# Kernel optimization log

Measured on AMD Instinct MI355X. Metric: run time of the kernel, lower is better.

Reference implementation:

```python
import jax, jax.numpy as jnp
import numpy as np

NUM_HEADS = 16
BLOCK_KV = 64


def _split_heads(x, h):
    B, T, D = x.shape
    return x.reshape(B, T, h, D // h).transpose(0, 2, 1, 3)  # [B,H,T,Hd]


def _merge_heads(x):
    B, H, T, Hd = x.shape
    return x.transpose(0, 2, 1, 3).reshape(B, T, H * Hd)


def _streaming_attention(qh, kh, vh, bkv):
    # Online-softmax (flash-attention) over kv blocks; math identical to the
    # original nested-loop version (including the Z + 1e-9 denominator).
    B, H, T, Dh = qh.shape
    scale = 1.0 / jnp.sqrt(Dh).astype(jnp.float32)
    q32 = qh.astype(jnp.float32)
    nb = T // bkv
    # [nb, B, H, bkv, Dh]
    kb = jnp.moveaxis(kh.astype(jnp.float32).reshape(B, H, nb, bkv, Dh), 2, 0)
    vb = jnp.moveaxis(vh.astype(jnp.float32).reshape(B, H, nb, bkv, Dh), 2, 0)

    def step(carry, blk):
        m, Z, O = carry
        k_blk, v_blk = blk
        scores = jnp.einsum('bhtd,bhkd->bhtk', q32, k_blk) * scale
        m_new = jnp.maximum(m, jnp.max(scores, axis=-1, keepdims=True))
        alpha = jnp.exp(m - m_new)
        p = jnp.exp(scores - m_new)
        Z = Z * alpha + jnp.sum(p, axis=-1, keepdims=True)
        O = O * alpha + jnp.einsum('bhtk,bhkd->bhtd', p, v_blk)
        return (m_new, Z, O), None

    m0 = jnp.full((B, H, T, 1), -jnp.inf, dtype=jnp.float32)
    Z0 = jnp.zeros((B, H, T, 1), dtype=jnp.float32)
    O0 = jnp.zeros((B, H, T, Dh), dtype=jnp.float32)
    (m, Z, O), _ = jax.lax.scan(step, (m0, Z0, O0), (kb, vb))
    return (O / (Z + 1e-9)).astype(qh.dtype)


def setup_inputs() -> dict:
    key = jax.random.key(0)
    ks = jax.random.split(key, 6)
    B, T, D = 4, 8192, 512
    s = 1.0 / np.sqrt(D)
    return {
        'x': jax.random.normal(ks[0], (B, T, D), dtype=jnp.float32),
        'Wq': jax.random.normal(ks[1], (D, D), dtype=jnp.float32) * s,
        'Wk': jax.random.normal(ks[2], (D, D), dtype=jnp.float32) * s,
        'Wv': jax.random.normal(ks[3], (D, D), dtype=jnp.float32) * s,
        'Wo': jax.random.normal(ks[4], (D, D), dtype=jnp.float32) * s,
        'bo': jnp.zeros((D,), dtype=jnp.float32),
    }


def reference(x, Wq, Wk, Wv, Wo, bo):
    q = x @ Wq
    k = x @ Wk
    v = x @ Wv
    qh = _split_heads(q, NUM_HEADS)
    kh = _split_heads(k, NUM_HEADS)
    vh = _split_heads(v, NUM_HEADS)
    out_h = _streaming_attention(qh, kh, vh, BLOCK_KV)
    return _merge_heads(out_h) @ Wo + bo
```

## Files before the change

### kernel.cpp

```cpp
#include <hip/hip_runtime.h>
#include <hip/hip_bf16.h>
#include <math.h>

typedef __bf16 bf16;
typedef __bf16 bf16x2 __attribute__((ext_vector_type(2)));
typedef __bf16 bf16x4 __attribute__((ext_vector_type(4)));
typedef __bf16 bf16x8 __attribute__((ext_vector_type(8)));
typedef float f32x4 __attribute__((ext_vector_type(4)));
typedef unsigned int u32;
typedef u32 u32x4 __attribute__((ext_vector_type(4)));

#define B_ 4
#define T_ 8192
#define D_ 512
#define H_ 16
#define HD_ 32
#define M_ (B_ * T_)

#if __has_builtin(__builtin_amdgcn_exp2f)
#define EXP2(x) __builtin_amdgcn_exp2f(x)
#else
#define EXP2(x) exp2f(x)
#endif

#define LDSP(p) ((__attribute__((address_space(3))) void*)(p))
#define GLBP(p) ((const __attribute__((address_space(1))) void*)(p))

static __device__ __forceinline__ u32 pkbf16(float a, float b) {
  bf16x2 t;
  t[0] = (bf16)a;
  t[1] = (bf16)b;
  return __builtin_bit_cast(u32, t);
}

static __device__ __forceinline__ void swap32(u32& a, u32& b) {
#if __has_builtin(__builtin_amdgcn_permlane32_swap)
  auto r = __builtin_amdgcn_permlane32_swap(a, b, false, false);
  a = r[0];
  b = r[1];
#else
  asm volatile("v_permlane32_swap_b32 %0, %1" : "+v"(a), "+v"(b));
#endif
}

__global__ void k_cvt(const float* __restrict__ in, bf16* __restrict__ out, int n4) {
  int i = blockIdx.x * blockDim.x + threadIdx.x;
  const int stride = gridDim.x * blockDim.x;
  for (; i < n4; i += stride) {
    const float4 v = ((const float4*)in)[i];
    bf16x4 o;
    o.x = (bf16)v.x; o.y = (bf16)v.y; o.z = (bf16)v.z; o.w = (bf16)v.w;
    ((bf16x4*)out)[i] = o;
  }
}

__global__ void k_cvt_T(const float* __restrict__ w, bf16* __restrict__ wT, float scale) {
  const int tid = blockIdx.x * blockDim.x + threadIdx.x;
  const int n = tid >> 9, k = tid & 511;
  wT[tid] = (bf16)(w[k * 512 + n] * scale);
}

__global__ __launch_bounds__(256) void k_transposeV(const bf16* __restrict__ V,
                                                    bf16* __restrict__ VT) {
  __shared__ bf16 tile[128][36];
  const int bh = blockIdx.y, chunk = blockIdx.x;
  const int b = bh >> 4, h = bh & 15;
  const int kv0 = chunk * 128;
  const int tid = threadIdx.x;
  const int r = tid >> 1, c0 = (tid & 1) * 16;
  const size_t ib = ((size_t)(b * T_ + kv0 + r)) * 512 + h * 32 + c0;
  *(bf16x8*)&tile[r][c0]     = *(const bf16x8*)&V[ib];
  *(bf16x8*)&tile[r][c0 + 8] = *(const bf16x8*)&V[ib + 8];
  __syncthreads();
  const int d = tid >> 3, j0 = (tid & 7) * 16;
  bf16x8 o0, o1;
#pragma unroll
  for (int i = 0; i < 4; ++i) {
    o0[i]     = tile[j0 + i][d];
    o0[i + 4] = tile[j0 + 8 + i][d];
    o1[i]     = tile[j0 + 4 + i][d];
    o1[i + 4] = tile[j0 + 12 + i][d];
  }
  const size_t ob = ((size_t)bh * 32 + d) * T_ + kv0 + j0;
  *(bf16x8*)&VT[ob] = o0;
  *(bf16x8*)&VT[ob + 8] = o1;
}

template <int OUTF32>
__global__ __launch_bounds__(256) void k_gemm(const bf16* __restrict__ A,
                                              const bf16* __restrict__ BT,
                                              void* __restrict__ Cout,
                                              const float* __restrict__ bias) {
  __shared__ bf16 As[128][40];
  __shared__ bf16 Bs[128][40];
  const int bn = blockIdx.x * 128;
  const int bm = blockIdx.y * 128;
  const int tid = threadIdx.x;
  const int l = tid & 63, wid = tid >> 6;
  const int ln = l & 15, ku = l >> 4;
  const int wm = (wid >> 1) * 64, wn = (wid & 1) * 64;
  const int sr = tid >> 2, sc = (tid & 3) * 8;

  f32x4 acc[4][4] = {};

  for (int ks = 0; ks < 512; ks += 32) {
    __syncthreads();
    *(bf16x8*)&As[sr][sc]      = *(const bf16x8*)&A[(size_t)(bm + sr) * 512 + ks + sc];
    *(bf16x8*)&As[sr + 64][sc] = *(const bf16x8*)&A[(size_t)(bm + sr + 64) * 512 + ks + sc];
    *(bf16x8*)&Bs[sr][sc]      = *(const bf16x8*)&BT[(size_t)(bn + sr) * 512 + ks + sc];
    *(bf16x8*)&Bs[sr + 64][sc] = *(const bf16x8*)&BT[(size_t)(bn + sr + 64) * 512 + ks + sc];
    __syncthreads();

    bf16x8 af[4], bfr[4];
#pragma unroll
    for (int mt = 0; mt < 4; ++mt) af[mt] = *(const bf16x8*)&As[wm + mt * 16 + ln][ku * 8];
#pragma unroll
    for (int nt = 0; nt < 4; ++nt) bfr[nt] = *(const bf16x8*)&Bs[wn + nt * 16 + ln][ku * 8];
#pragma unroll
    for (int mt = 0; mt < 4; ++mt)
#pragma unroll
      for (int nt = 0; nt < 4; ++nt)
        acc[mt][nt] = __builtin_amdgcn_mfma_f32_16x16x32_bf16(af[mt], bfr[nt], acc[mt][nt], 0, 0, 0);
  }

#pragma unroll
  for (int mt = 0; mt < 4; ++mt)
#pragma unroll
    for (int nt = 0; nt < 4; ++nt)
#pragma unroll
      for (int r = 0; r < 4; ++r) {
        const int row = bm + wm + mt * 16 + ku * 4 + r;
        const int col = bn + wn + nt * 16 + ln;
        const float v = acc[mt][nt][r];
        if (OUTF32)
          ((float*)Cout)[(size_t)row * 512 + col] = v + bias[col];
        else
          ((bf16*)Cout)[(size_t)row * 512 + col] = (bf16)v;
      }
}

__global__ __launch_bounds__(256, 5) void k_attn(const bf16* __restrict__ Q,
                                                 const bf16* __restrict__ K,
                                                 const bf16* __restrict__ VT,
                                                 bf16* __restrict__ O) {
  __shared__ bf16 ks[2][64][32];
  __shared__ bf16 vts[2][32][64];
  const int qt = blockIdx.x;
  const int bh = blockIdx.y;
  const int b = bh >> 4, h = bh & 15;
  const size_t base = (size_t)b * T_ * 512 + (size_t)h * 32;
  const size_t vtbase = (size_t)bh * 32 * T_;
  const int tid = threadIdx.x;
  const int l = tid & 63, w = tid >> 6;
  const int ln = l & 15, ku = l >> 4;

  const int q0 = qt * 128 + w * 32;
  bf16x8 qf[2];
#pragma unroll
  for (int j = 0; j < 2; ++j)
    qf[j] = *(const bf16x8*)&Q[base + (size_t)(q0 + j * 16 + ln) * 512 + ku * 8];

  const u32 one2 = 0x3F803F80u;
  u32x4 onesu = {one2, one2, one2, one2};
  const bf16x8 ones = __builtin_bit_cast(bf16x8, onesu);

  const int krow = tid >> 2;
  const int kchS = ((tid & 3) ^ ((krow >> 1) & 3)) * 8;
  const int vrow = tid >> 3;
  const int vchS = ((tid & 7) ^ (vrow & 7)) * 8;
  const bf16* gk = K + base + (size_t)krow * 512 + kchS;
  const bf16* gv = VT + vtbase + (size_t)vrow * T_ + vchS;

  bf16* dk0 = &ks[0][w * 16][0];
  bf16* dk1 = &ks[1][w * 16][0];
  bf16* dv0 = &vts[0][w * 8][0];
  bf16* dv1 = &vts[1][w * 8][0];

  const char* ksr = (const char*)&ks[0][0][0] + ln * 64 + 16 * (ku ^ ((ln >> 1) & 3));
  const char* vr0 = (const char*)&vts[0][0][0] + ln * 128 + 16 * ((ku) ^ (ln & 7));
  const char* vr1 = (const char*)&vts[0][0][0] + ln * 128 + 16 * ((4 + ku) ^ (ln & 7));

  f32x4 o[2][2] = {};
  f32x4 zacc[2] = {};

  __builtin_amdgcn_global_load_lds(GLBP(gk), LDSP(dk0), 16, 0, 0);
  __builtin_amdgcn_global_load_lds(GLBP(gv), LDSP(dv0), 16, 0, 0);
  gk += 64 * 512;
  gv += 64;
  __syncthreads();

#define KV_BODY(CUR, DKN, DVN)                                                        \
  {                                                                                   \
    __builtin_amdgcn_global_load_lds(GLBP(gk), LDSP(DKN), 16, 0, 0);                  \
    __builtin_amdgcn_global_load_lds(GLBP(gv), LDSP(DVN), 16, 0, 0);                  \
    gk += 64 * 512;                                                                   \
    gv += 64;                                                                         \
    _Pragma("unroll") for (int j = 0; j < 2; ++j) {                                   \
      _Pragma("unroll") for (int c = 0; c < 2; ++c) {                                 \
        const bf16x8 kf0 = *(const bf16x8*)(ksr + (CUR)*4096 + c * 2048);             \
        const bf16x8 kf1 = *(const bf16x8*)(ksr + (CUR)*4096 + c * 2048 + 1024);      \
        const f32x4 zz = {};                                                          \
        f32x4 s0 = __builtin_amdgcn_mfma_f32_16x16x32_bf16(kf0, qf[j], zz, 0, 0, 0);  \
        f32x4 s1 = __builtin_amdgcn_mfma_f32_16x16x32_bf16(kf1, qf[j], zz, 0, 0, 0);  \
        u32 lo0 = pkbf16(EXP2(s0[0]), EXP2(s0[1]));                                   \
        u32 hi0 = pkbf16(EXP2(s0[2]), EXP2(s0[3]));                                   \
        u32 lo1 = pkbf16(EXP2(s1[0]), EXP2(s1[1]));                                   \
        u32 hi1 = pkbf16(EXP2(s1[2]), EXP2(s1[3]));                                   \
        swap32(lo0, lo1);                                                             \
        swap32(hi0, hi1);                                                             \
        u32x4 pd = {lo0, hi0, lo1, hi1};                                              \
        const bf16x8 pf = __builtin_bit_cast(bf16x8, pd);                             \
        const bf16x8 va0 =                                                            \
            *(const bf16x8*)((c ? vr1 : vr0) + (CUR)*4096);                           \
        const bf16x8 va1 =                                                            \
            *(const bf16x8*)((c ? vr1 : vr0) + (CUR)*4096 + 2048);                    \
        o[j][0] = __builtin_amdgcn_mfma_f32_16x16x32_bf16(va0, pf, o[j][0], 0, 0, 0); \
        o[j][1] = __builtin_amdgcn_mfma_f32_16x16x32_bf16(va1, pf, o[j][1], 0, 0, 0); \
        zacc[j] = __builtin_amdgcn_mfma_f32_16x16x32_bf16(ones, pf, zacc[j], 0, 0, 0);\
      }                                                                               \
    }                                                                                 \
    __syncthreads();                                                                  \
  }

  for (int kb = 0; kb < 128; kb += 2) {
    KV_BODY(0, dk1, dv1);
    KV_BODY(1, dk0, dv0);
  }
#undef KV_BODY

#pragma unroll
  for (int j = 0; j < 2; ++j) {
    const float iz = 1.0f / (zacc[j][0] + 1e-9f);
    bf16x4 w0, w1;
#pragma unroll
    for (int r = 0; r < 4; ++r) {
      w0[r] = (bf16)(o[j][0][r] * iz);
      w1[r] = (bf16)(o[j][1][r] * iz);
    }
    const size_t row = base + (size_t)(q0 + j * 16 + ln) * 512;
    *(bf16x4*)&O[row + ku * 4] = w0;
    *(bf16x4*)&O[row + 16 + ku * 4] = w1;
  }
}

extern "C" void kernel_launch(void* const* d_in, const int* in_sizes, int n_in,
                              void* d_out, int out_size, void* d_ws, size_t ws_size,
                              hipStream_t stream) {
  const float* x = (const float*)d_in[0];
  const float* Wq = (const float*)d_in[1];
  const float* Wk = (const float*)d_in[2];
  const float* Wv = (const float*)d_in[3];
  const float* Wo = (const float*)d_in[4];
  const float* bo = (const float*)d_in[5];
  float* out = (float*)d_out;

  char* ws = (char*)d_ws;
  const size_t SZ = (size_t)M_ * 512 * sizeof(bf16);
  bf16* xb = (bf16*)(ws);
  bf16* qb = (bf16*)(ws + SZ);
  bf16* kb = (bf16*)(ws + 2 * SZ);
  bf16* vb = (bf16*)(ws + 3 * SZ);
  bf16* ob = (bf16*)(ws + 4 * SZ);
  bf16* wqT = (bf16*)(ws + 5 * SZ);
  bf16* wkT = wqT + 512 * 512;
  bf16* wvT = wkT + 512 * 512;
  bf16* woT = wvT + 512 * 512;
  bf16* vt = xb;

  const float SCALE_L2E = 0.17677669529663687f * 1.4426950408889634f;

  k_cvt<<<2048, 256, 0, stream>>>(x, xb, M_ * 512 / 4);
  k_cvt_T<<<1024, 256, 0, stream>>>(Wq, wqT, SCALE_L2E);
  k_cvt_T<<<1024, 256, 0, stream>>>(Wk, wkT, 1.0f);
  k_cvt_T<<<1024, 256, 0, stream>>>(Wv, wvT, 1.0f);
  k_cvt_T<<<1024, 256, 0, stream>>>(Wo, woT, 1.0f);

  dim3 gg(4, 256);
  k_gemm<0><<<gg, 256, 0, stream>>>(xb, wqT, qb, nullptr);
  k_gemm<0><<<gg, 256, 0, stream>>>(xb, wkT, kb, nullptr);
  k_gemm<0><<<gg, 256, 0, stream>>>(xb, wvT, vb, nullptr);

  dim3 gt(64, 64);
  k_transposeV<<<gt, 256, 0, stream>>>(vb, vt);
  dim3 ga(64, 64);
  k_attn<<<ga, 256, 0, stream>>>(qb, kb, vt, ob);

  k_gemm<1><<<gg, 256, 0, stream>>>(ob, woT, out, bo);
}
```

Before: 832.6 us.

## Use triple-buffered LDS ring with explicit vmcnt waits in attention kernel

The attention KV loop moves from a double-buffered scheme with a full __syncthreads after each block to a three-slot LDS ring. Prefetches run two blocks ahead, and each step does a partial s_waitcnt vmcnt plus an s_barrier before computing. This gives the async global-to-LDS loads more time in flight and drops the full LDS/VM drain that __syncthreads implies. In exchange, LDS use per block rises by half, which may lower occupancy at 5 blocks per CU. It also relies on hand-written wait counts and sched_barrier placement being correct.

```diff
diff --git a/kernel.cpp b/kernel.cpp
--- a/kernel.cpp
+++ b/kernel.cpp
@@ -143,8 +143,8 @@
                                                  const bf16* __restrict__ K,
                                                  const bf16* __restrict__ VT,
                                                  bf16* __restrict__ O) {
-  __shared__ bf16 ks[2][64][32];
-  __shared__ bf16 vts[2][32][64];
+  __shared__ bf16 ks[3][64][32];
+  __shared__ bf16 vts[3][32][64];
   const int qt = blockIdx.x;
   const int bh = blockIdx.y;
   const int b = bh >> 4, h = bh & 15;
@@ -171,10 +171,8 @@
   const bf16* gk = K + base + (size_t)krow * 512 + kchS;
   const bf16* gv = VT + vtbase + (size_t)vrow * T_ + vchS;
 
-  bf16* dk0 = &ks[0][w * 16][0];
-  bf16* dk1 = &ks[1][w * 16][0];
-  bf16* dv0 = &vts[0][w * 8][0];
-  bf16* dv1 = &vts[1][w * 8][0];
+  bf16* const dk[3] = {&ks[0][w * 16][0], &ks[1][w * 16][0], &ks[2][w * 16][0]};
+  bf16* const dv[3] = {&vts[0][w * 8][0], &vts[1][w * 8][0], &vts[2][w * 8][0]};
 
   const char* ksr = (const char*)&ks[0][0][0] + ln * 64 + 16 * (ku ^ ((ln >> 1) & 3));
   const char* vr0 = (const char*)&vts[0][0][0] + ln * 128 + 16 * ((ku) ^ (ln & 7));
@@ -183,50 +181,59 @@
   f32x4 o[2][2] = {};
   f32x4 zacc[2] = {};
 
-  __builtin_amdgcn_global_load_lds(GLBP(gk), LDSP(dk0), 16, 0, 0);
-  __builtin_amdgcn_global_load_lds(GLBP(gv), LDSP(dv0), 16, 0, 0);
+  __builtin_amdgcn_global_load_lds(GLBP(gk), LDSP(dk[0]), 16, 0, 0);
+  __builtin_amdgcn_global_load_lds(GLBP(gv), LDSP(dv[0]), 16, 0, 0);
   gk += 64 * 512;
   gv += 64;
-  __syncthreads();
-
-#define KV_BODY(CUR, DKN, DVN)                                                        \
-  {                                                                                   \
-    __builtin_amdgcn_global_load_lds(GLBP(gk), LDSP(DKN), 16, 0, 0);                  \
-    __builtin_amdgcn_global_load_lds(GLBP(gv), LDSP(DVN), 16, 0, 0);                  \
-    gk += 64 * 512;                                                                   \
-    gv += 64;                                                                         \
-    _Pragma("unroll") for (int j = 0; j < 2; ++j) {                                   \
-      _Pragma("unroll") for (int c = 0; c < 2; ++c) {                                 \
-        const bf16x8 kf0 = *(const bf16x8*)(ksr + (CUR)*4096 + c * 2048);             \
-        const bf16x8 kf1 = *(const bf16x8*)(ksr + (CUR)*4096 + c * 2048 + 1024);      \
-        const f32x4 zz = {};                                                          \
-        f32x4 s0 = __builtin_amdgcn_mfma_f32_16x16x32_bf16(kf0, qf[j], zz, 0, 0, 0);  \
-        f32x4 s1 = __builtin_amdgcn_mfma_f32_16x16x32_bf16(kf1, qf[j], zz, 0, 0, 0);  \
-        u32 lo0 = pkbf16(EXP2(s0[0]), EXP2(s0[1]));                                   \
-        u32 hi0 = pkbf16(EXP2(s0[2]), EXP2(s0[3]));                                   \
-        u32 lo1 = pkbf16(EXP2(s1[0]), EXP2(s1[1]));                                   \
-        u32 hi1 = pkbf16(EXP2(s1[2]), EXP2(s1[3]));                                   \
-        swap32(lo0, lo1);                                                             \
-        swap32(hi0, hi1);                                                             \
-        u32x4 pd = {lo0, hi0, lo1, hi1};                                              \
-        const bf16x8 pf = __builtin_bit_cast(bf16x8, pd);                             \
-        const bf16x8 va0 =                                                            \
-            *(const bf16x8*)((c ? vr1 : vr0) + (CUR)*4096);                           \
-        const bf16x8 va1 =                                                            \
-            *(const bf16x8*)((c ? vr1 : vr0) + (CUR)*4096 + 2048);                    \
-        o[j][0] = __builtin_amdgcn_mfma_f32_16x16x32_bf16(va0, pf, o[j][0], 0, 0, 0); \
-        o[j][1] = __builtin_amdgcn_mfma_f32_16x16x32_bf16(va1, pf, o[j][1], 0, 0, 0); \
-        zacc[j] = __builtin_amdgcn_mfma_f32_16x16x32_bf16(ones, pf, zacc[j], 0, 0, 0);\
-      }                                                                               \
-    }                                                                                 \
-    __syncthreads();                                                                  \
-  }
-
-  for (int kb = 0; kb < 128; kb += 2) {
-    KV_BODY(0, dk1, dv1);
-    KV_BODY(1, dk0, dv0);
-  }
-#undef KV_BODY
+  __builtin_amdgcn_global_load_lds(GLBP(gk), LDSP(dk[1]), 16, 0, 0);
+  __builtin_amdgcn_global_load_lds(GLBP(gv), LDSP(dv[1]), 16, 0, 0);
+  gk += 64 * 512;
+  gv += 64;
+
+#define KV_RING(SLOT_C, SLOT_S, VM, STG)                                                \
+  {                                                                                     \
+    asm volatile("s_waitcnt vmcnt(" VM ")" ::: "memory");                               \
+    __builtin_amdgcn_sched_barrier(0);                                                  \
+    __builtin_amdgcn_s_barrier();                                                       \
+    __builtin_amdgcn_sched_barrier(0);                                                  \
+    if (STG) {                                                                          \
+      __builtin_amdgcn_global_load_lds(GLBP(gk), LDSP(dk[SLOT_S]), 16, 0, 0);           \
+      __builtin_amdgcn_global_load_lds(GLBP(gv), LDSP(dv[SLOT_S]), 16, 0, 0);           \
+      gk += 64 * 512;                                                                   \
+      gv += 64;                                                                         \
+    }                                                                                   \
+    _Pragma("unroll") for (int j = 0; j < 2; ++j) {                                     \
+      _Pragma("unroll") for (int c = 0; c < 2; ++c) {                                   \
+        const bf16x8 kf0 = *(const bf16x8*)(ksr + (SLOT_C)*4096 + c * 2048);            \
+        const bf16x8 kf1 = *(const bf16x8*)(ksr + (SLOT_C)*4096 + c * 2048 + 1024);     \
+        const f32x4 zz = {};                                                            \
+        f32x4 s0 = __builtin_amdgcn_mfma_f32_16x16x32_bf16(kf0, qf[j], zz, 0, 0, 0);    \
+        f32x4 s1 = __builtin_amdgcn_mfma_f32_16x16x32_bf16(kf1, qf[j], zz, 0, 0, 0);    \
+        u32 lo0 = pkbf16(EXP2(s0[0]), EXP2(s0[1]));                                     \
+        u32 hi0 = pkbf16(EXP2(s0[2]), EXP2(s0[3]));                                     \
+        u32 lo1 = pkbf16(EXP2(s1[0]), EXP2(s1[1]));                                     \
+        u32 hi1 = pkbf16(EXP2(s1[2]), EXP2(s1[3]));                                     \
+        swap32(lo0, lo1);                                                               \
+        swap32(hi0, hi1);                                                               \
+        u32x4 pd = {lo0, hi0, lo1, hi1};                                                \
+        const bf16x8 pf = __builtin_bit_cast(bf16x8, pd);                               \
+        const bf16x8 va0 = *(const bf16x8*)((c ? vr1 : vr0) + (SLOT_C)*4096);           \
+        const bf16x8 va1 = *(const bf16x8*)((c ? vr1 : vr0) + (SLOT_C)*4096 + 2048);    \
+        o[j][0] = __builtin_amdgcn_mfma_f32_16x16x32_bf16(va0, pf, o[j][0], 0, 0, 0);   \
+        o[j][1] = __builtin_amdgcn_mfma_f32_16x16x32_bf16(va1, pf, o[j][1], 0, 0, 0);   \
+        zacc[j] = __builtin_amdgcn_mfma_f32_16x16x32_bf16(ones, pf, zacc[j], 0, 0, 0);  \
+      }                                                                                 \
+    }                                                                                   \
+  }
+
+  for (int it = 0; it < 42; ++it) {
+    KV_RING(0, 2, "2", 1);
+    KV_RING(1, 0, "2", 1);
+    KV_RING(2, 1, "2", 1);
+  }
+  KV_RING(0, 2, "2", 0);
+  KV_RING(1, 0, "0", 0);
+#undef KV_RING
 
 #pragma unroll
   for (int j = 0; j < 2; ++j) {
```

New measurement: 828.5 us. No clear change (-0.5%).
